# Optimization experiments

Hardware: AMD Instinct MI355X
Metric: run time of the kernel (lower is better)

The kernel has to match this reference:

```python
import jax, jax.numpy as jnp
import numpy as np

B, N, D = 4, 1024, 1024
H, HD = 16, 64  # num_heads, head_dim


def rotate_half(x):
    x1, x2 = jnp.split(x, 2, axis=-1)
    return jnp.concatenate([-x2, x1], axis=-1)


def setup_inputs() -> dict:
    key = jax.random.key(0)
    ks = jax.random.split(key, 10)
    s = 1.0 / np.sqrt(D)
    hidden_states = jax.random.normal(ks[0], (B, N, D), jnp.float32)
    # rotary angles -> cos/sin per position per head-dim
    ang = jax.random.uniform(ks[1], (B, N, HD), jnp.float32, 0.0, 2 * np.pi)
    cos, sin = jnp.cos(ang), jnp.sin(ang)
    wq = jax.random.normal(ks[2], (D, D), jnp.float32) * s
    bq = jnp.zeros((D,), jnp.float32)
    wk = jax.random.normal(ks[3], (D, D), jnp.float32) * s  # key_bias=False
    wv = jax.random.normal(ks[4], (D, D), jnp.float32) * s
    bv = jnp.zeros((D,), jnp.float32)
    wo = jax.random.normal(ks[5], (D, D), jnp.float32) * s
    bo = jnp.zeros((D,), jnp.float32)
    return {"hidden_states": hidden_states, "cos": cos, "sin": sin,
            "wq": wq, "bq": bq, "wk": wk, "wv": wv, "bv": bv,
            "wo": wo, "bo": bo}


def reference(hidden_states, cos, sin, wq, bq, wk, wv, bv, wo, bo):
    # weights are (out, in) as in eqx Linear: y = x @ W.T + b
    q = jnp.einsum('bnd,ed->bne', hidden_states, wq) + bq
    k = jnp.einsum('bnd,ed->bne', hidden_states, wk)
    v = jnp.einsum('bnd,ed->bne', hidden_states, wv) + bv
    # [B, H, N, HD]
    q = q.reshape(B, N, H, HD).transpose(0, 2, 1, 3)
    k = k.reshape(B, N, H, HD).transpose(0, 2, 1, 3)
    v = v.reshape(B, N, H, HD).transpose(0, 2, 1, 3)
    c = cos[:, None, :, :]  # broadcast over heads
    s = sin[:, None, :, :]
    q = q * c + rotate_half(q) * s
    k = k * c + rotate_half(k) * s
    scale = 1.0 / np.sqrt(HD)
    scores = jnp.einsum('bhqd,bhkd->bhqk', q, k) * scale
    attn = jax.nn.softmax(scores, axis=-1)
    out = jnp.einsum('bhqk,bhkd->bhqd', attn, v)
    out = out.transpose(0, 2, 1, 3).reshape(B, N, D)
    return jnp.einsum('bnd,ed->bne', out, wo) + bo
```

## Files before the change

kernel.cpp:

```cpp
#include <hip/hip_runtime.h>
#include <hip/hip_bf16.h>
#include <cstdint>


typedef _Float16 half8 __attribute__((ext_vector_type(8)));
typedef _Float16 half4 __attribute__((ext_vector_type(4)));
typedef float f32x4 __attribute__((ext_vector_type(4)));

#define DEV_INLINE __device__ __forceinline__

constexpr int Bb = 4, Ns = 1024, Dd = 1024, Hh = 16, HDd = 64;
constexpr int M_ROWS = Bb * Ns;
constexpr int EQKV = 3 * Dd;

constexpr size_t OFF_HSH  = 0;
constexpr size_t SZ_HSH   = (size_t)M_ROWS * Dd * 2;
constexpr size_t OFF_WQKV = OFF_HSH + SZ_HSH;
constexpr size_t SZ_WQKV  = (size_t)EQKV * Dd * 2;
constexpr size_t OFF_WO   = OFF_WQKV + SZ_WQKV;
constexpr size_t SZ_WO    = (size_t)Dd * Dd * 2;
constexpr size_t OFF_BIAS = OFF_WO + SZ_WO;
constexpr size_t OFF_ATTN = OFF_BIAS + 16384;
constexpr size_t SZ_HEADS = (size_t)Bb * Hh * Ns * HDd * 2;
constexpr size_t OFF_QT   = OFF_ATTN + SZ_HEADS;
constexpr size_t OFF_KT   = OFF_QT + SZ_HEADS;
constexpr size_t OFF_VT   = OFF_KT + SZ_HEADS;

DEV_INLINE void async_cp16(const _Float16* g, _Float16* l) {
  __builtin_amdgcn_global_load_lds(
      (const __attribute__((address_space(1))) unsigned int*)(g),
      (__attribute__((address_space(3))) unsigned int*)(l), 16, 0, 0);
}

DEV_INLINE half4 cvt4(float4 v) {
  half4 h;
  h[0] = (_Float16)v.x; h[1] = (_Float16)v.y;
  h[2] = (_Float16)v.z; h[3] = (_Float16)v.w;
  return h;
}

__global__ __launch_bounds__(256) void cvt_kernel(
    const float* __restrict__ hs, const float* __restrict__ wq,
    const float* __restrict__ wk, const float* __restrict__ wv,
    const float* __restrict__ wo, const float* __restrict__ bq,
    const float* __restrict__ bv, _Float16* __restrict__ hsH,
    _Float16* __restrict__ wqkvH, _Float16* __restrict__ woH,
    float* __restrict__ biasP)
{
  const int gid = blockIdx.x * 256 + threadIdx.x;
  const int nHs4 = M_ROWS * Dd / 4;
  const int nW4  = 3 * Dd * Dd / 4;
  const int nWo4 = Dd * Dd / 4;
  if (gid < EQKV / 4) {
#pragma unroll
    for (int j = 0; j < 4; ++j) {
      int e = gid * 4 + j;
      biasP[e] = (e < 1024) ? bq[e] : (e < 2048 ? 0.f : bv[e - 2048]);
    }
  }
  if (gid < nHs4) {
    float4 v = reinterpret_cast<const float4*>(hs)[gid];
    reinterpret_cast<half4*>(hsH)[gid] = cvt4(v);
  } else if (gid < nHs4 + nW4) {
    int j = gid - nHs4;
    const int per = Dd * Dd / 4;
    const float* src = (j < per) ? wq : (j < 2 * per ? wk : wv);
    float4 v = reinterpret_cast<const float4*>(src)[j % per];
    reinterpret_cast<half4*>(wqkvH)[j] = cvt4(v);
  } else if (gid < nHs4 + nW4 + nWo4) {
    int j = gid - nHs4 - nW4;
    float4 v = reinterpret_cast<const float4*>(wo)[j];
    reinterpret_cast<half4*>(woH)[j] = cvt4(v);
  }
}

__global__ __launch_bounds__(512, 2) void gemm_qkv8(
    const _Float16* __restrict__ A, const _Float16* __restrict__ Bt,
    const float* __restrict__ bias, _Float16* __restrict__ vTo,
    const float* __restrict__ cosp, const float* __restrict__ sinp,
    _Float16* __restrict__ qT, _Float16* __restrict__ kT)
{
  __shared__ _Float16 AsP[4 * 256 * 32];
  __shared__ _Float16 BsP[4 * 256 * 32];
  constexpr int Kc = 1024;
  const int t = threadIdx.x;
  const int lane = t & 63, wave = t >> 6;
  const int c = lane & 15, g = lane >> 4;
  const int wm = wave >> 2, wn = wave & 3;
  const int m0 = blockIdx.y * 256, e0 = blockIdx.x * 256;

  const int scol8 = ((t & 3) ^ ((t >> 3) & 3)) * 8;
  const _Float16* gA0 = A  + (size_t)(m0 + (t >> 2)) * Kc + scol8;
  const _Float16* gB0 = Bt + (size_t)(e0 + (t >> 2)) * Kc + scol8;
  char* ldsA = (char*)AsP;
  char* ldsB = (char*)BsP;
  const int wb = wave * 1024;

  auto stage = [&](int tt) {
    char* la = ldsA + (tt & 3) * 16384 + wb;
    char* lb = ldsB + (tt & 3) * 16384 + wb;
    const _Float16* ga = gA0 + tt * 32;
    const _Float16* gb = gB0 + tt * 32;
    async_cp16(ga, (_Float16*)la);
    async_cp16(ga + (size_t)128 * Kc, (_Float16*)(la + 8192));
    async_cp16(gb, (_Float16*)lb);
    async_cp16(gb + (size_t)128 * Kc, (_Float16*)(lb + 8192));
  };

  const int swz16 = (g ^ ((c >> 1) & 3)) << 4;
  const int offA0 = (wm * 128 + c) * 64 + swz16;
  const int offB0 = (wn * 64 + c) * 64 + swz16;

  f32x4 acc[8][4];
  const f32x4 zero = {0.f, 0.f, 0.f, 0.f};
#pragma unroll
  for (int mi = 0; mi < 8; ++mi)
#pragma unroll
    for (int j = 0; j < 4; ++j) acc[mi][j] = zero;

  stage(0); stage(1); stage(2);

  for (int tt = 0; tt < 32; ++tt) {
    __builtin_amdgcn_s_barrier();
    if (tt < 30)       asm volatile("s_waitcnt vmcnt(8)" ::: "memory");
    else if (tt == 30) asm volatile("s_waitcnt vmcnt(4)" ::: "memory");
    else               asm volatile("s_waitcnt vmcnt(0)" ::: "memory");
    if (tt < 29) stage(tt + 3);

    const char* bA = ldsA + (tt & 3) * 16384;
    const char* bB = ldsB + (tt & 3) * 16384;
    half8 bf[4];
#pragma unroll
    for (int j = 0; j < 4; ++j)
      bf[j] = *reinterpret_cast<const half8*>(bB + offB0 + j * 1024);
    __builtin_amdgcn_s_setprio(1);
#pragma unroll
    for (int mi = 0; mi < 8; ++mi) {
      half8 a = *reinterpret_cast<const half8*>(bA + offA0 + mi * 1024);
#pragma unroll
      for (int j = 0; j < 4; ++j)
        acc[mi][j] = __builtin_amdgcn_mfma_f32_16x16x32_f16(a, bf[j], acc[mi][j], 0, 0, 0);
    }
    __builtin_amdgcn_s_setprio(0);
  }

  const int scol = e0 + wn * 64;
  const int sec = scol >> 10;
  const int h = (scol & 1023) >> 6;
  const int bh = (m0 >> 10) * Hh + h;
  if (sec < 2) {
    _Float16* dst = sec ? kT : qT;
#pragma unroll
    for (int mi = 0; mi < 8; ++mi)
#pragma unroll
      for (int r = 0; r < 4; ++r) {
        int row = m0 + wm * 128 + mi * 16 + g * 4 + r;
        size_t obase = ((size_t)bh * Ns + (row & 1023)) * HDd;
        const float* cb = cosp + (size_t)row * HDd;
        const float* sb = sinp + (size_t)row * HDd;
#pragma unroll
        for (int j = 0; j < 2; ++j) {
          int hd = j * 16 + c;
          float x1 = acc[mi][j][r]     + bias[scol + hd];
          float x2 = acc[mi][j + 2][r] + bias[scol + hd + 32];
          float c1 = cb[hd],      s1 = sb[hd];
          float c2 = cb[hd + 32], s2 = sb[hd + 32];
          dst[obase + hd]      = (_Float16)(x1 * c1 - x2 * s1);
          dst[obase + hd + 32] = (_Float16)(x2 * c2 + x1 * s2);
        }
      }
  } else {
    _Float16* vbase = vTo + (size_t)bh * (HDd * Ns) + (m0 & 1023) + wm * 128;
#pragma unroll
    for (int mi = 0; mi < 8; ++mi)
#pragma unroll
      for (int j = 0; j < 4; ++j) {
        int hd = j * 16 + c;
        float bv_ = bias[scol + hd];
        half4 pk;
#pragma unroll
        for (int r = 0; r < 4; ++r) pk[r] = (_Float16)(acc[mi][j][r] + bv_);
        *reinterpret_cast<half4*>(vbase + (size_t)hd * Ns + mi * 16 + g * 4) = pk;
      }
  }
}

__global__ __launch_bounds__(256, 3) void gemm_out(
    const _Float16* __restrict__ A, const _Float16* __restrict__ Bt,
    const float* __restrict__ bias, float* __restrict__ out,
    int M, int E, int K)
{
  constexpr int BN = 64, JW = 2;
  __shared__ _Float16 As[128 * 64];
  __shared__ _Float16 Bs[BN * 64];
  const int t = threadIdx.x;
  const int lane = t & 63, wave = t >> 6;
  const int c15 = lane & 15, g = lane >> 4;
  const int wm = wave >> 1, wn = wave & 1;
  const int m0 = blockIdx.y * 128, e0 = blockIdx.x * BN;

  const int srow  = t >> 3;
  const int scol8 = ((t & 7) ^ ((t >> 3) & 7)) * 8;
  const _Float16* gA0 = A  + (size_t)(m0 + srow) * K + scol8;
  const _Float16* gB0 = Bt + (size_t)(e0 + srow) * K + scol8;
  char* lA = (char*)As + wave * 1024;
  char* lB = (char*)Bs + wave * 1024;

  const char* pA[4][2];
  const char* pB[JW][2];
#pragma unroll
  for (int mi = 0; mi < 4; ++mi)
#pragma unroll
    for (int kh = 0; kh < 2; ++kh) {
      int ra = wm * 64 + mi * 16 + c15;
      pA[mi][kh] = (const char*)As + ra * 128 + (((kh * 4 + g) ^ (ra & 7)) << 4);
    }
#pragma unroll
  for (int j = 0; j < JW; ++j)
#pragma unroll
    for (int kh = 0; kh < 2; ++kh) {
      int rb = wn * (BN / 2) + j * 16 + c15;
      pB[j][kh] = (const char*)Bs + rb * 128 + (((kh * 4 + g) ^ (rb & 7)) << 4);
    }

  f32x4 acc[4][JW];
  const f32x4 zero = {0.f, 0.f, 0.f, 0.f};
#pragma unroll
  for (int i = 0; i < 4; ++i)
#pragma unroll
    for (int j = 0; j < JW; ++j) acc[i][j] = zero;

  const int nk = K >> 6;
  for (int kt = 0; kt < nk; ++kt) {
    const _Float16* ga = gA0 + kt * 64;
    const _Float16* gb = gB0 + kt * 64;
#pragma unroll
    for (int i = 0; i < 4; ++i)
      async_cp16(ga + (size_t)(32 * i) * K, (_Float16*)(lA + i * 4096));
#pragma unroll
    for (int i = 0; i < BN / 32; ++i)
      async_cp16(gb + (size_t)(32 * i) * K, (_Float16*)(lB + i * 4096));
    __syncthreads();
#pragma unroll
    for (int kh = 0; kh < 2; ++kh) {
      half8 a[4], b[JW];
#pragma unroll
      for (int i = 0; i < 4; ++i) a[i] = *reinterpret_cast<const half8*>(pA[i][kh]);
#pragma unroll
      for (int j = 0; j < JW; ++j) b[j] = *reinterpret_cast<const half8*>(pB[j][kh]);
#pragma unroll
      for (int i = 0; i < 4; ++i)
#pragma unroll
        for (int j = 0; j < JW; ++j)
          acc[i][j] = __builtin_amdgcn_mfma_f32_16x16x32_f16(a[i], b[j], acc[i][j], 0, 0, 0);
    }
    __syncthreads();
  }

#pragma unroll
  for (int i = 0; i < 4; ++i)
#pragma unroll
    for (int j = 0; j < JW; ++j)
#pragma unroll
      for (int r = 0; r < 4; ++r) {
        int row = m0 + wm * 64 + i * 16 + g * 4 + r;
        int col = e0 + wn * (BN / 2) + j * 16 + c15;
        out[(size_t)row * E + col] = acc[i][j][r] + bias[col];
      }
}

__global__ __launch_bounds__(256, 2) void attn_kernel(
    const _Float16* __restrict__ qT, const _Float16* __restrict__ kT,
    const _Float16* __restrict__ vT, _Float16* __restrict__ attnH)
{
  __shared__ _Float16 Ks[2][64 * 64];
  __shared__ _Float16 Vst[2][64 * 64];
  __shared__ _Float16 Ps[128 * 64];
  const int t = threadIdx.x;
  const int lane = t & 63, wave = t >> 6;
  const int c = lane & 15, g = lane >> 4;
  const int bx = blockIdx.x;
  const int qt = bx & 7, bh = bx >> 3;
  const int b = bh >> 4, h = bh & 15;
  const int qn0 = qt * 128;
  const int wq0 = wave * 32;

  half8 qf[2][2];
#pragma unroll
  for (int s16 = 0; s16 < 2; ++s16) {
    const _Float16* qp =
        qT + ((size_t)bh * Ns + qn0 + wq0 + s16 * 16 + c) * HDd + g * 8;
    qf[s16][0] = *reinterpret_cast<const half8*>(qp);
    qf[s16][1] = *reinterpret_cast<const half8*>(qp + 32);
  }

  half8 ones;
#pragma unroll
  for (int j = 0; j < 8; ++j) ones[j] = (_Float16)1.0f;

  f32x4 accO[2][4];
  f32x4 accL[2];
  const f32x4 zero = {0.f, 0.f, 0.f, 0.f};
#pragma unroll
  for (int s16 = 0; s16 < 2; ++s16) {
    accL[s16] = zero;
#pragma unroll
    for (int d = 0; d < 4; ++d) accO[s16][d] = zero;
  }

  const int srow = t >> 3, sch = t & 7;
  const int ssw = (sch * 16) ^ ((srow & 7) << 4);
  const _Float16* gK = kT + ((size_t)bh * Ns + srow) * HDd + sch * 8;
  const _Float16* gV = vT + ((size_t)bh * HDd + srow) * Ns + sch * 8;
  char* wKa = (char*)Ks[0]  + srow * 128 + ssw;
  char* wVa = (char*)Vst[0] + srow * 128 + ssw;

  const char* pK[2][4];
  const char* pV[2][4];
  const char* pP[2][2];
#pragma unroll
  for (int ks = 0; ks < 2; ++ks) {
#pragma unroll
    for (int i = 0; i < 4; ++i) {
      int rowk = i * 16 + c;
      pK[ks][i] = (const char*)Ks[0]  + rowk * 128 + ((ks * 64 + g * 16) ^ ((rowk & 7) << 4));
      pV[ks][i] = (const char*)Vst[0] + rowk * 128 + ((ks * 64 + g * 16) ^ ((rowk & 7) << 4));
    }
#pragma unroll
    for (int s16 = 0; s16 < 2; ++s16) {
      int rowp = wq0 + s16 * 16 + c;
      pP[s16][ks] = (const char*)Ps + rowp * 128 + ((ks * 64 + g * 16) ^ ((rowp & 7) << 4));
    }
  }

  const float K1 = 0.18033688011112042f;
  const float K2 = -11.541560327111707f;
  char* prow0 = (char*)Ps + (wq0 + c) * 128;
  const int psw = (c & 7) << 4;

  {
    half8 k0 = *reinterpret_cast<const half8*>(gK);
    half8 k1 = *reinterpret_cast<const half8*>(gK + 32 * HDd);
    half8 v0 = *reinterpret_cast<const half8*>(gV);
    half8 v1 = *reinterpret_cast<const half8*>(gV + 32 * Ns);
    *reinterpret_cast<half8*>(wKa) = k0;
    *reinterpret_cast<half8*>(wKa + 4096) = k1;
    *reinterpret_cast<half8*>(wVa) = v0;
    *reinterpret_cast<half8*>(wVa + 4096) = v1;
  }
  __syncthreads();

  for (int jt = 0; jt < 16; ++jt) {
    const int bo = (jt & 1) * 8192;
    const bool pre = (jt + 1 < 16);
    half8 kr0, kr1, vr0, vr1;
    if (pre) {
      kr0 = *reinterpret_cast<const half8*>(gK + (jt + 1) * 4096);
      kr1 = *reinterpret_cast<const half8*>(gK + (jt + 1) * 4096 + 32 * HDd);
      vr0 = *reinterpret_cast<const half8*>(gV + (jt + 1) * 64);
      vr1 = *reinterpret_cast<const half8*>(gV + (jt + 1) * 64 + 32 * Ns);
    }

    f32x4 s[2][4];
#pragma unroll
    for (int s16 = 0; s16 < 2; ++s16)
#pragma unroll
      for (int i = 0; i < 4; ++i) s[s16][i] = zero;
    __builtin_amdgcn_s_setprio(1);
#pragma unroll
    for (int ks = 0; ks < 2; ++ks) {
      half8 kf[4];
#pragma unroll
      for (int i = 0; i < 4; ++i)
        kf[i] = *reinterpret_cast<const half8*>(pK[ks][i] + bo);
#pragma unroll
      for (int i = 0; i < 4; ++i) {
        s[0][i] = __builtin_amdgcn_mfma_f32_16x16x32_f16(kf[i], qf[0][ks], s[0][i], 0, 0, 0);
        s[1][i] = __builtin_amdgcn_mfma_f32_16x16x32_f16(kf[i], qf[1][ks], s[1][i], 0, 0, 0);
      }
    }
    __builtin_amdgcn_s_setprio(0);

#pragma unroll
    for (int s16 = 0; s16 < 2; ++s16) {
      char* prow = prow0 + s16 * 2048;
#pragma unroll
      for (int i = 0; i < 4; ++i) {
        half4 pk;
        pk[0] = (_Float16)__builtin_amdgcn_exp2f(fmaf(s[s16][i][0], K1, K2));
        pk[1] = (_Float16)__builtin_amdgcn_exp2f(fmaf(s[s16][i][1], K1, K2));
        pk[2] = (_Float16)__builtin_amdgcn_exp2f(fmaf(s[s16][i][2], K1, K2));
        pk[3] = (_Float16)__builtin_amdgcn_exp2f(fmaf(s[s16][i][3], K1, K2));
        *reinterpret_cast<half4*>(prow + ((i * 32 + g * 8) ^ psw)) = pk;
      }
    }

    __builtin_amdgcn_s_setprio(1);
#pragma unroll
    for (int ks = 0; ks < 2; ++ks) {
      half8 pa0 = *reinterpret_cast<const half8*>(pP[0][ks]);
      half8 pa1 = *reinterpret_cast<const half8*>(pP[1][ks]);
      accL[0] = __builtin_amdgcn_mfma_f32_16x16x32_f16(pa0, ones, accL[0], 0, 0, 0);
      accL[1] = __builtin_amdgcn_mfma_f32_16x16x32_f16(pa1, ones, accL[1], 0, 0, 0);
#pragma unroll
      for (int dt = 0; dt < 4; ++dt) {
        half8 vf = *reinterpret_cast<const half8*>(pV[ks][dt] + bo);
        accO[0][dt] = __builtin_amdgcn_mfma_f32_16x16x32_f16(pa0, vf, accO[0][dt], 0, 0, 0);
        accO[1][dt] = __builtin_amdgcn_mfma_f32_16x16x32_f16(pa1, vf, accO[1][dt], 0, 0, 0);
      }
    }
    __builtin_amdgcn_s_setprio(0);

    if (pre) {
      const int wo_ = 8192 - bo;
      *reinterpret_cast<half8*>(wKa + wo_) = kr0;
      *reinterpret_cast<half8*>(wKa + wo_ + 4096) = kr1;
      *reinterpret_cast<half8*>(wVa + wo_) = vr0;
      *reinterpret_cast<half8*>(wVa + wo_ + 4096) = vr1;
      __syncthreads();
    }
  }

#pragma unroll
  for (int s16 = 0; s16 < 2; ++s16)
#pragma unroll
    for (int r = 0; r < 4; ++r) {
      float inv = 1.f / accL[s16][r];
      int n = qn0 + wq0 + s16 * 16 + g * 4 + r;
#pragma unroll
      for (int dt = 0; dt < 4; ++dt) {
        float v = accO[s16][dt][r] * inv;
        attnH[((size_t)b * Ns + n) * Dd + h * HDd + dt * 16 + c] = (_Float16)v;
      }
    }
}

extern "C" void kernel_launch(void* const* d_in, const int* in_sizes, int n_in,
                              void* d_out, int out_size, void* d_ws, size_t ws_size,
                              hipStream_t stream) {
  const float* hs   = (const float*)d_in[0];
  const float* cosp = (const float*)d_in[1];
  const float* sinp = (const float*)d_in[2];
  const float* wq   = (const float*)d_in[3];
  const float* bq   = (const float*)d_in[4];
  const float* wk   = (const float*)d_in[5];
  const float* wv   = (const float*)d_in[6];
  const float* bv   = (const float*)d_in[7];
  const float* wo   = (const float*)d_in[8];
  const float* bo   = (const float*)d_in[9];

  char* ws = (char*)d_ws;
  _Float16* hsH   = (_Float16*)(ws + OFF_HSH);
  _Float16* wqkvH = (_Float16*)(ws + OFF_WQKV);
  _Float16* woH   = (_Float16*)(ws + OFF_WO);
  float*    biasP = (float*)(ws + OFF_BIAS);
  _Float16* attnH = (_Float16*)(ws + OFF_ATTN);
  _Float16* qTp   = (_Float16*)(ws + OFF_QT);
  _Float16* kTp   = (_Float16*)(ws + OFF_KT);
  _Float16* vTp   = (_Float16*)(ws + OFF_VT);

  cvt_kernel<<<8192, 256, 0, stream>>>(hs, wq, wk, wv, wo, bq, bv,
                                       hsH, wqkvH, woH, biasP);
  gemm_qkv8<<<dim3(EQKV / 256, M_ROWS / 256), 512, 0, stream>>>(
      hsH, wqkvH, biasP, vTp, cosp, sinp, qTp, kTp);
  attn_kernel<<<Bb * Hh * (Ns / 128), 256, 0, stream>>>(qTp, kTp, vTp, attnH);
  gemm_out<<<dim3(Dd / 64, M_ROWS / 128), 256, 0, stream>>>(
      attnH, woH, bo, (float*)d_out, M_ROWS, Dd, Dd);
}
```

Measured before the change: 110.5 us.

## Replace 256x256 pipelined QKV GEMM with 128x128 two-wave tiles; reorder attention blocks

The QKV projection GEMM drops its 8-wave, 256x256-tile kernel with a 4-stage async pipeline. In its place is a 2-wave, 128x128-tile kernel that loads a full 64-wide K slice per iteration with XOR-swizzled LDS and synchronizes twice per step with no prefetch overlap. Each wave now computes a 128x64 output, and the grid grows to 4x more blocks. The attention kernel's block index mapping is also swapped so consecutive blocks cover different (batch, head) pairs instead of different query tiles. The change trades pipelining and per-block reuse for more blocks and simpler synchronization, which risks exposing global load latency.

```diff
diff --git a/kernel.cpp b/kernel.cpp
--- a/kernel.cpp
+++ b/kernel.cpp
@@ -74,42 +74,43 @@
   }
 }
 
-__global__ __launch_bounds__(512, 2) void gemm_qkv8(
+__global__ __launch_bounds__(128, 2) void gemm_qkv(
     const _Float16* __restrict__ A, const _Float16* __restrict__ Bt,
     const float* __restrict__ bias, _Float16* __restrict__ vTo,
     const float* __restrict__ cosp, const float* __restrict__ sinp,
     _Float16* __restrict__ qT, _Float16* __restrict__ kT)
 {
-  __shared__ _Float16 AsP[4 * 256 * 32];
-  __shared__ _Float16 BsP[4 * 256 * 32];
   constexpr int Kc = 1024;
+  __shared__ _Float16 As[128 * 64];
+  __shared__ _Float16 Bs[128 * 64];
   const int t = threadIdx.x;
-  const int lane = t & 63, wave = t >> 6;
+  const int lane = t & 63, w = t >> 6;
   const int c = lane & 15, g = lane >> 4;
-  const int wm = wave >> 2, wn = wave & 3;
-  const int m0 = blockIdx.y * 256, e0 = blockIdx.x * 256;
-
-  const int scol8 = ((t & 3) ^ ((t >> 3) & 3)) * 8;
-  const _Float16* gA0 = A  + (size_t)(m0 + (t >> 2)) * Kc + scol8;
-  const _Float16* gB0 = Bt + (size_t)(e0 + (t >> 2)) * Kc + scol8;
-  char* ldsA = (char*)AsP;
-  char* ldsB = (char*)BsP;
-  const int wb = wave * 1024;
-
-  auto stage = [&](int tt) {
-    char* la = ldsA + (tt & 3) * 16384 + wb;
-    char* lb = ldsB + (tt & 3) * 16384 + wb;
-    const _Float16* ga = gA0 + tt * 32;
-    const _Float16* gb = gB0 + tt * 32;
-    async_cp16(ga, (_Float16*)la);
-    async_cp16(ga + (size_t)128 * Kc, (_Float16*)(la + 8192));
-    async_cp16(gb, (_Float16*)lb);
-    async_cp16(gb + (size_t)128 * Kc, (_Float16*)(lb + 8192));
-  };
-
-  const int swz16 = (g ^ ((c >> 1) & 3)) << 4;
-  const int offA0 = (wm * 128 + c) * 64 + swz16;
-  const int offB0 = (wn * 64 + c) * 64 + swz16;
+  const int m0 = blockIdx.y * 128, e0 = blockIdx.x * 128;
+
+  const int srow  = t >> 3;
+  const int scol8 = ((t & 7) ^ ((t >> 3) & 7)) * 8;
+  const _Float16* gA0 = A  + (size_t)(m0 + srow) * Kc + scol8;
+  const _Float16* gB0 = Bt + (size_t)(e0 + srow) * Kc + scol8;
+  char* lA = (char*)As + t * 16;
+  char* lB = (char*)Bs + t * 16;
+
+  const char* pA[8][2];
+  const char* pB[4][2];
+#pragma unroll
+  for (int mi = 0; mi < 8; ++mi)
+#pragma unroll
+    for (int kh = 0; kh < 2; ++kh) {
+      int ra = mi * 16 + c;
+      pA[mi][kh] = (const char*)As + ra * 128 + (((kh * 4 + g) ^ (ra & 7)) << 4);
+    }
+#pragma unroll
+  for (int j = 0; j < 4; ++j)
+#pragma unroll
+    for (int kh = 0; kh < 2; ++kh) {
+      int rb = w * 64 + j * 16 + c;
+      pB[j][kh] = (const char*)Bs + rb * 128 + (((kh * 4 + g) ^ (rb & 7)) << 4);
+    }
 
   f32x4 acc[8][4];
   const f32x4 zero = {0.f, 0.f, 0.f, 0.f};
@@ -118,33 +119,32 @@
 #pragma unroll
     for (int j = 0; j < 4; ++j) acc[mi][j] = zero;
 
-  stage(0); stage(1); stage(2);
-
-  for (int tt = 0; tt < 32; ++tt) {
-    __builtin_amdgcn_s_barrier();
-    if (tt < 30)       asm volatile("s_waitcnt vmcnt(8)" ::: "memory");
-    else if (tt == 30) asm volatile("s_waitcnt vmcnt(4)" ::: "memory");
-    else               asm volatile("s_waitcnt vmcnt(0)" ::: "memory");
-    if (tt < 29) stage(tt + 3);
-
-    const char* bA = ldsA + (tt & 3) * 16384;
-    const char* bB = ldsB + (tt & 3) * 16384;
-    half8 bf[4];
-#pragma unroll
-    for (int j = 0; j < 4; ++j)
-      bf[j] = *reinterpret_cast<const half8*>(bB + offB0 + j * 1024);
-    __builtin_amdgcn_s_setprio(1);
-#pragma unroll
-    for (int mi = 0; mi < 8; ++mi) {
-      half8 a = *reinterpret_cast<const half8*>(bA + offA0 + mi * 1024);
-#pragma unroll
-      for (int j = 0; j < 4; ++j)
-        acc[mi][j] = __builtin_amdgcn_mfma_f32_16x16x32_f16(a, bf[j], acc[mi][j], 0, 0, 0);
-    }
-    __builtin_amdgcn_s_setprio(0);
-  }
-
-  const int scol = e0 + wn * 64;
+  for (int kt = 0; kt < 16; ++kt) {
+    const _Float16* ga = gA0 + kt * 64;
+    const _Float16* gb = gB0 + kt * 64;
+#pragma unroll
+    for (int i = 0; i < 8; ++i) {
+      async_cp16(ga + (size_t)(16 * i) * Kc, (_Float16*)(lA + i * 2048));
+      async_cp16(gb + (size_t)(16 * i) * Kc, (_Float16*)(lB + i * 2048));
+    }
+    __syncthreads();
+#pragma unroll
+    for (int kh = 0; kh < 2; ++kh) {
+      half8 b[4];
+#pragma unroll
+      for (int j = 0; j < 4; ++j) b[j] = *reinterpret_cast<const half8*>(pB[j][kh]);
+#pragma unroll
+      for (int mi = 0; mi < 8; ++mi) {
+        half8 a = *reinterpret_cast<const half8*>(pA[mi][kh]);
+#pragma unroll
+        for (int j = 0; j < 4; ++j)
+          acc[mi][j] = __builtin_amdgcn_mfma_f32_16x16x32_f16(a, b[j], acc[mi][j], 0, 0, 0);
+      }
+    }
+    __syncthreads();
+  }
+
+  const int scol = e0 + w * 64;
   const int sec = scol >> 10;
   const int h = (scol & 1023) >> 6;
   const int bh = (m0 >> 10) * Hh + h;
@@ -154,7 +154,7 @@
     for (int mi = 0; mi < 8; ++mi)
 #pragma unroll
       for (int r = 0; r < 4; ++r) {
-        int row = m0 + wm * 128 + mi * 16 + g * 4 + r;
+        int row = m0 + mi * 16 + g * 4 + r;
         size_t obase = ((size_t)bh * Ns + (row & 1023)) * HDd;
         const float* cb = cosp + (size_t)row * HDd;
         const float* sb = sinp + (size_t)row * HDd;
@@ -170,7 +170,7 @@
         }
       }
   } else {
-    _Float16* vbase = vTo + (size_t)bh * (HDd * Ns) + (m0 & 1023) + wm * 128;
+    _Float16* vbase = vTo + (size_t)bh * (HDd * Ns) + (m0 & 1023);
 #pragma unroll
     for (int mi = 0; mi < 8; ++mi)
 #pragma unroll
@@ -280,7 +280,7 @@
   const int lane = t & 63, wave = t >> 6;
   const int c = lane & 15, g = lane >> 4;
   const int bx = blockIdx.x;
-  const int qt = bx & 7, bh = bx >> 3;
+  const int qt = bx >> 6, bh = bx & 63;
   const int b = bh >> 4, h = bh & 15;
   const int qn0 = qt * 128;
   const int wq0 = wave * 32;
@@ -461,7 +461,7 @@
 
   cvt_kernel<<<8192, 256, 0, stream>>>(hs, wq, wk, wv, wo, bq, bv,
                                        hsH, wqkvH, woH, biasP);
-  gemm_qkv8<<<dim3(EQKV / 256, M_ROWS / 256), 512, 0, stream>>>(
+  gemm_qkv<<<dim3(EQKV / 128, M_ROWS / 128), 128, 0, stream>>>(
       hsH, wqkvH, biasP, vTp, cosp, sinp, qTp, kTp);
   attn_kernel<<<Bb * Hh * (Ns / 128), 256, 0, stream>>>(qTp, kTp, vTp, attnH);
   gemm_out<<<dim3(Dd / 64, M_ROWS / 128), 256, 0, stream>>>(
```

Result: faster. 94.53 us (-14.4%).
